# Kernel tuning notes

Hardware: AMD Instinct MI355X
Metric: run time of the kernel (lower is better)

The kernel has to match this reference:

```python
import jax, jax.numpy as jnp
import numpy as np
from jax import lax

GO = 1  # mead-baseline Offsets.GO
NEG = -10000.0


def setup_inputs() -> dict:
    key = jax.random.key(0)
    k1, k2, k3, k4 = jax.random.split(key, 4)
    B, T, K = 1024, 512, 64
    unary = jax.random.normal(k1, (B, T, K), dtype=jnp.float32)
    lengths = jax.random.randint(k2, (B,), 1, T + 1).astype(jnp.int32)
    inv_mask = jax.random.randint(k3, (K, K), 0, 2).astype(jnp.int32)
    A = (jax.random.normal(k4, (K, K), dtype=jnp.float32) * 0.1)
    return {"unary": unary, "lengths": lengths, "inv_mask": inv_mask, "A": A}


def _viterbi(probv, trans, seq_lens):
    """Masked Viterbi decode (tf.contrib.crf.crf_decode semantics).

    probv: [B, T1, K] unary scores (GO frame already prepended)
    trans: [K, K] transition scores, trans[i, j] = score(i -> j)
    seq_lens: [B] int32, valid lengths (already +1 for the GO frame)
    """
    B, T1, K = probv.shape
    alpha0 = probv[:, 0]                      # [B, K]
    us = jnp.swapaxes(probv[:, 1:], 0, 1)     # [T1-1, B, K]
    ts = jnp.arange(1, T1)

    def fwd(alpha, xs):
        u_t, t = xs
        scores = alpha[:, :, None] + trans[None]        # [B, K_prev, K_cur]
        bp = jnp.argmax(scores, axis=1).astype(jnp.int32)  # [B, K]
        new_alpha = jnp.max(scores, axis=1) + u_t
        alpha = jnp.where((t < seq_lens)[:, None], new_alpha, alpha)  # freeze past length
        return alpha, bp

    alpha_f, bps = lax.scan(fwd, alpha0, (us, ts))  # bps: [T1-1, B, K]
    last = jnp.argmax(alpha_f, axis=-1).astype(jnp.int32)  # [B] tag at last valid step
    best = jnp.max(alpha_f, axis=-1)                       # [B]

    def bwd(tag, xs):
        bp_t, t = xs
        prev = jnp.take_along_axis(bp_t, tag[:, None], axis=1)[:, 0]
        prev = jnp.where(t < seq_lens, prev, tag)  # beyond length: carry tag back
        return prev, prev

    _, prevs = lax.scan(bwd, last, (bps[::-1], ts[::-1]))  # prevs: [T1-1, B] (times T1-2..0)
    tags = jnp.concatenate([prevs[::-1], last[None]], axis=0)  # [T1, B]
    return jnp.swapaxes(tags, 0, 1), best


def reference(unary, lengths, inv_mask, A):
    B, T, K = unary.shape
    inv = inv_mask.astype(jnp.float32) * NEG
    trans = jax.nn.log_softmax(A + inv, axis=-1)
    gos = jnp.full((1, 1, K), NEG, dtype=unary.dtype).at[:, :, GO].set(0.0)
    probv = jnp.concatenate([jnp.broadcast_to(gos, (B, 1, K)), unary], axis=1)  # [B, T+1, K]
    viterbi, _ = _viterbi(probv, trans, lengths.astype(jnp.int32) + 1)
    return viterbi[:, 1:]  # drop GO position -> [B, T]
```

## Files before the change

### kernel.cpp

```cpp
#include <hip/hip_runtime.h>

#define NEGV -10000.0f
#define BB 1024
#define TT 512
#define KK 64

typedef float vf2 __attribute__((ext_vector_type(2)));

#define BAR() asm volatile("s_waitcnt lgkmcnt(0)\n\ts_barrier" ::: "memory")

__global__ __launch_bounds__(64)
void trans_kernel(const float* __restrict__ A, const int* __restrict__ inv,
                  float* __restrict__ trans)
{
    const int i = blockIdx.x, j = threadIdx.x;
    float x = A[i * KK + j] + (inv[i * KK + j] ? NEGV : 0.0f);
    float m = x;
    #pragma unroll
    for (int o = 32; o > 0; o >>= 1) m = fmaxf(m, __shfl_xor(m, o));
    float e = expf(x - m);
    float s = e;
    #pragma unroll
    for (int o = 32; o > 0; o >>= 1) s += __shfl_xor(s, o);
    trans[i * KK + j] = (x - m) - logf(s);
}


#define FILL4(BUF_, RB_)                                                       \
  { _Pragma("unroll")                                                          \
    for (int d_ = 0; d_ < 4; ++d_) {                                           \
        int r_ = (RB_) + d_; if (r_ > TT - 1) r_ = TT - 1;                     \
        BUF_[d_] = ur[r_ * KK + lane];                                         \
    } }

#define STEP(T_, UV_)                                                          \
  {                                                                            \
                       \
    float sv[32];                                                              \
    _Pragma("unroll")                                                          \
    for (int q = 0; q < 8; ++q) {                                              \
        vf2 t01 = vf2{a4[q].x, a4[q].y} + Tr2[2 * q];                          \
        vf2 t23 = vf2{a4[q].z, a4[q].w} + Tr2[2 * q + 1];                      \
        sv[4 * q + 0] = t01.x; sv[4 * q + 1] = t01.y;                          \
        sv[4 * q + 2] = t23.x; sv[4 * q + 3] = t23.y;                          \
    }                                                                          \
                      \
    float l0[11];                                                              \
    _Pragma("unroll")                                                          \
    for (int i = 0; i < 10; ++i)                                               \
        l0[i] = fmaxf(fmaxf(sv[3 * i], sv[3 * i + 1]), sv[3 * i + 2]);         \
    l0[10] = fmaxf(sv[30], sv[31]);                                            \
    float l1a = fmaxf(fmaxf(l0[0], l0[1]), l0[2]);                             \
    float l1b = fmaxf(fmaxf(l0[3], l0[4]), l0[5]);                             \
    float l1c = fmaxf(fmaxf(l0[6], l0[7]), l0[8]);                             \
    float l1d = fmaxf(l0[9], l0[10]);                                          \
    float mw  = fmaxf(fmaxf(fmaxf(l1a, l1b), l1c), l1d);                       \
                   \
    int idx = 31;                                                              \
    _Pragma("unroll")                                                          \
    for (int i = 30; i >= 0; --i) idx = (sv[i] == mw) ? i : idx;               \
    if (wv == 1) {                                                             \
        int2 pk; pk.x = __float_as_int(mw); pk.y = idx + 32;                   \
        sMI[lane] = pk;                                                        \
    }                                                                          \
    BAR();                                    \
    if (wv == 0) {                                                             \
        int2 pk = sMI[lane];                                                   \
        float m1 = __int_as_float(pk.x);                                       \
        float m  = fmaxf(mw, m1);                                              \
        int  bpi = (m1 > mw) ? pk.y : idx;       \
        float u_ = (UV_);                                                      \
        asm volatile("" : "+v"(u_));                                           \
        if ((T_) <= len) alpha = m + u_;                                       \
        sA[lane] = alpha;                                                      \
        if ((T_) >= 2 && (T_) <= len)                                          \
            sbp[((T_) - 2) * KK + lane] = (unsigned char)bpi;                  \
    }                                                                          \
    BAR();                                    \
    {                                                                          \
        const float4* p = (const float4*)sA + wv * 8;                          \
        _Pragma("unroll")                                                      \
        for (int q = 0; q < 8; ++q) a4[q] = p[q];                              \
    }                                                                          \
  }

__global__ __launch_bounds__(128, 1)
void viterbi_kernel(const float* __restrict__ unary, const int* __restrict__ lengths,
                    const float* __restrict__ trans, int* __restrict__ out)
{
    const int tid  = threadIdx.x;
    const int wv   = tid >> 6;
    const int lane = tid & 63;
    const int b    = blockIdx.x;

    __shared__ unsigned char sbp[(TT - 1) * KK];
    __shared__ float sA[KK];
    __shared__ int2  sMI[KK];

    vf2 Tr2[16];
    #pragma unroll
    for (int q = 0; q < 16; ++q) {
        Tr2[q].x = trans[(wv * 32 + 2 * q)     * KK + lane];
        Tr2[q].y = trans[(wv * 32 + 2 * q + 1) * KK + lane];
    }

    const int len = lengths[b];
    const float* ur = unary + (long)b * (TT * KK);
    int* orow = out + b * TT;

    float ub0[4], ub1[4];
    if (wv == 0) { FILL4(ub0, 0) FILL4(ub1, 4) }

    float alpha = (lane == 1) ? 0.0f : NEGV;
    if (wv == 0) sA[lane] = alpha;
    BAR();

    float4 a4[8];
    {
        const float4* p = (const float4*)sA + wv * 8;
        #pragma unroll
        for (int q = 0; q < 8; ++q) a4[q] = p[q];
    }

    for (int tb = 1; tb <= len; tb += 8) {
        STEP(tb + 0, ub0[0]) STEP(tb + 1, ub0[1])
        STEP(tb + 2, ub0[2]) STEP(tb + 3, ub0[3])
        if (wv == 0) FILL4(ub0, tb + 7)
        STEP(tb + 4, ub1[0]) STEP(tb + 5, ub1[1])
        STEP(tb + 6, ub1[2]) STEP(tb + 7, ub1[3])
        if (wv == 0) FILL4(ub1, tb + 11)
    }

    if (wv == 1) return;

    float mm = alpha;
    #pragma unroll
    for (int o = 32; o > 0; o >>= 1) mm = fmaxf(mm, __shfl_xor(mm, o));
    unsigned long long msk = __ballot(alpha == mm);
    int last = __ffsll(msk) - 1;

    for (int jj = len - 1 + lane; jj < TT; jj += 64) orow[jj] = last;

    asm volatile("s_waitcnt lgkmcnt(0)" ::: "memory");

    int tag = last;
    for (int t = len; t >= 2; --t) {
        int prev = sbp[(t - 2) * KK + tag];
        if (lane == 0) orow[t - 2] = prev;
        tag = prev;
    }
}

extern "C" void kernel_launch(void* const* d_in, const int* in_sizes, int n_in,
                              void* d_out, int out_size, void* d_ws, size_t ws_size,
                              hipStream_t stream)
{
    const float* unary   = (const float*)d_in[0];
    const int*   lengths = (const int*)d_in[1];
    const int*   inv     = (const int*)d_in[2];
    const float* A       = (const float*)d_in[3];
    int*         out     = (int*)d_out;

    float* trans = (float*)d_ws;

    trans_kernel<<<KK, KK, 0, stream>>>(A, inv, trans);
    viterbi_kernel<<<BB, 128, 0, stream>>>(unary, lengths, trans, out);
}
```

Before: 452.7 us.

## Split reduction across lane halves with shuffle merge, one barrier per step

Reassigns work so each wave covers 32 current-state columns, with each half-wave reducing over 32 previous states. The two halves are merged with a cross-lane shuffle instead of a shared-memory exchange, which removes one of the two block barriers per time step. The first-index argmax tie-break is kept through an index-min tree and a >= / > comparison. Launch bounds now allow two blocks per CU to improve occupancy, and both waves load unary values; the low half writes alpha while the high half writes backpointers.

```diff
diff --git a/kernel.cpp b/kernel.cpp
--- a/kernel.cpp
+++ b/kernel.cpp
@@ -26,16 +26,18 @@
 }
 
 
+__device__ __forceinline__ int imin3(int a, int b, int c) { return min(min(a, b), c); }
+
 #define FILL4(BUF_, RB_)                                                       \
   { _Pragma("unroll")                                                          \
     for (int d_ = 0; d_ < 4; ++d_) {                                           \
         int r_ = (RB_) + d_; if (r_ > TT - 1) r_ = TT - 1;                     \
-        BUF_[d_] = ur[r_ * KK + lane];                                         \
+        BUF_[d_] = ur[r_ * KK + j];                                            \
     } }
 
 #define STEP(T_, UV_)                                                          \
   {                                                                            \
-                       \
+                      \
     float sv[32];                                                              \
     _Pragma("unroll")                                                          \
     for (int q = 0; q < 8; ++q) {                                              \
@@ -44,7 +46,7 @@
         sv[4 * q + 0] = t01.x; sv[4 * q + 1] = t01.y;                          \
         sv[4 * q + 2] = t23.x; sv[4 * q + 3] = t23.y;                          \
     }                                                                          \
-                      \
+                                          \
     float l0[11];                                                              \
     _Pragma("unroll")                                                          \
     for (int i = 0; i < 10; ++i)                                               \
@@ -55,53 +57,61 @@
     float l1c = fmaxf(fmaxf(l0[6], l0[7]), l0[8]);                             \
     float l1d = fmaxf(l0[9], l0[10]);                                          \
     float mw  = fmaxf(fmaxf(fmaxf(l1a, l1b), l1c), l1d);                       \
-                   \
-    int idx = 31;                                                              \
+       \
+    int c[32];                                                                 \
     _Pragma("unroll")                                                          \
-    for (int i = 30; i >= 0; --i) idx = (sv[i] == mw) ? i : idx;               \
-    if (wv == 1) {                                                             \
-        int2 pk; pk.x = __float_as_int(mw); pk.y = idx + 32;                   \
-        sMI[lane] = pk;                                                        \
-    }                                                                          \
-    BAR();                                    \
-    if (wv == 0) {                                                             \
-        int2 pk = sMI[lane];                                                   \
-        float m1 = __int_as_float(pk.x);                                       \
-        float m  = fmaxf(mw, m1);                                              \
-        int  bpi = (m1 > mw) ? pk.y : idx;       \
-        float u_ = (UV_);                                                      \
-        asm volatile("" : "+v"(u_));                                           \
-        if ((T_) <= len) alpha = m + u_;                                       \
-        sA[lane] = alpha;                                                      \
-        if ((T_) >= 2 && (T_) <= len)                                          \
-            sbp[((T_) - 2) * KK + lane] = (unsigned char)bpi;                  \
-    }                                                                          \
-    BAR();                                    \
+    for (int i = 0; i < 32; ++i) c[i] = (sv[i] == mw) ? i : 32;                \
+    int n0[11];                                                                \
+    _Pragma("unroll")                                                          \
+    for (int i = 0; i < 10; ++i)                                               \
+        n0[i] = imin3(c[3 * i], c[3 * i + 1], c[3 * i + 2]);                   \
+    n0[10] = min(c[30], c[31]);                                                \
+    int n1a = imin3(n0[0], n0[1], n0[2]);                                      \
+    int n1b = imin3(n0[3], n0[4], n0[5]);                                      \
+    int n1c = imin3(n0[6], n0[7], n0[8]);                                      \
+    int n1d = min(n0[9], n0[10]);                                              \
+    int gidx = min(min(min(n1a, n1b), n1c), n1d) + ibase;                      \
+     \
+    float mo = __shfl_xor(mw, 32);                                             \
+    int   go = __shfl_xor(gidx, 32);                                           \
+    bool take = ishi ? (mo >= mw) : (mo > mw);                                 \
+    float m  = fmaxf(mw, mo);                                                  \
+    int  bpi = take ? go : gidx;                                               \
+    float u_ = (UV_);                                                          \
+    asm volatile("" : "+v"(u_));                                               \
+    if ((T_) <= len) alpha = m + u_;         \
+    if (!ishi) sA[j] = alpha;                  \
+    else if ((T_) >= 2 && (T_) <= len)                                         \
+        sbp[((T_) - 2) * KK + j] = (unsigned char)bpi;       \
+    BAR();             \
     {                                                                          \
-        const float4* p = (const float4*)sA + wv * 8;                          \
+        const float4* p = (const float4*)sA + (ibase >> 2);                    \
         _Pragma("unroll")                                                      \
         for (int q = 0; q < 8; ++q) a4[q] = p[q];                              \
     }                                                                          \
   }
 
-__global__ __launch_bounds__(128, 1)
+__global__ __launch_bounds__(128, 2)
 void viterbi_kernel(const float* __restrict__ unary, const int* __restrict__ lengths,
                     const float* __restrict__ trans, int* __restrict__ out)
 {
-    const int tid  = threadIdx.x;
-    const int wv   = tid >> 6;
-    const int lane = tid & 63;
-    const int b    = blockIdx.x;
+    const int tid   = threadIdx.x;
+    const int wv    = tid >> 6;
+    const int lane  = tid & 63;
+    const int sub   = lane & 31;
+    const int ibase = (lane >> 5) << 5;
+    const bool ishi = (lane >= 32);
+    const int j     = wv * 32 + sub;
+    const int b     = blockIdx.x;
 
     __shared__ unsigned char sbp[(TT - 1) * KK];
-    __shared__ float sA[KK];
-    __shared__ int2  sMI[KK];
+    __shared__ __align__(16) float sA[KK];
 
     vf2 Tr2[16];
     #pragma unroll
     for (int q = 0; q < 16; ++q) {
-        Tr2[q].x = trans[(wv * 32 + 2 * q)     * KK + lane];
-        Tr2[q].y = trans[(wv * 32 + 2 * q + 1) * KK + lane];
+        Tr2[q].x = trans[(ibase + 2 * q)     * KK + j];
+        Tr2[q].y = trans[(ibase + 2 * q + 1) * KK + j];
     }
 
     const int len = lengths[b];
@@ -109,15 +119,15 @@
     int* orow = out + b * TT;
 
     float ub0[4], ub1[4];
-    if (wv == 0) { FILL4(ub0, 0) FILL4(ub1, 4) }
+    FILL4(ub0, 0) FILL4(ub1, 4)
 
-    float alpha = (lane == 1) ? 0.0f : NEGV;
-    if (wv == 0) sA[lane] = alpha;
+    float alpha = (j == 1) ? 0.0f : NEGV;
+    if (!ishi) sA[j] = alpha;
     BAR();
 
     float4 a4[8];
     {
-        const float4* p = (const float4*)sA + wv * 8;
+        const float4* p = (const float4*)sA + (ibase >> 2);
         #pragma unroll
         for (int q = 0; q < 8; ++q) a4[q] = p[q];
     }
@@ -125,18 +135,19 @@
     for (int tb = 1; tb <= len; tb += 8) {
         STEP(tb + 0, ub0[0]) STEP(tb + 1, ub0[1])
         STEP(tb + 2, ub0[2]) STEP(tb + 3, ub0[3])
-        if (wv == 0) FILL4(ub0, tb + 7)
+        FILL4(ub0, tb + 7)
         STEP(tb + 4, ub1[0]) STEP(tb + 5, ub1[1])
         STEP(tb + 6, ub1[2]) STEP(tb + 7, ub1[3])
-        if (wv == 0) FILL4(ub1, tb + 11)
+        FILL4(ub1, tb + 11)
     }
 
     if (wv == 1) return;
 
-    float mm = alpha;
+    float av = sA[lane];
+    float mm = av;
     #pragma unroll
     for (int o = 32; o > 0; o >>= 1) mm = fmaxf(mm, __shfl_xor(mm, o));
-    unsigned long long msk = __ballot(alpha == mm);
+    unsigned long long msk = __ballot(av == mm);
     int last = __ffsll(msk) - 1;
 
     for (int jj = len - 1 + lane; jj < TT; jj += 64) orow[jj] = last;
```

New measurement: 440.9 us. -2.6%, faster.
